# Performance work log

Hardware: AMD Instinct MI355X
Metric: run time of the kernel (lower is better)

The kernel has to match this reference:

```python
import jax, jax.numpy as jnp
import numpy as np

N_CODEBOOKS = 4
N_EMBED = 1024
EMBED_DIM = 64
PATCH = 4
BETA = 0.25
EPS = 1e-5
USAGE_W = 0.01


def setup_inputs() -> dict:
    key = jax.random.key(0)
    k1, k2 = jax.random.split(key)
    z = jax.random.normal(k1, (8, 64, 128, 128), dtype=jnp.float32)
    # one EMA codebook per quantizer, initialized ~ randn like torch buffer
    codebooks = jax.random.normal(k2, (N_CODEBOOKS, N_EMBED, EMBED_DIM), dtype=jnp.float32)
    return {"z": z, "codebooks": codebooks}


def _usage_loss(indices, n_embed):
    # negative-entropy penalty on code usage (no gradient path: counts are ints)
    counts = jnp.bincount(indices.reshape(-1), length=n_embed).astype(jnp.float32)
    probs = (counts + EPS) / (counts.sum() + EPS * n_embed)
    entropy = -jnp.sum(probs * jnp.log(probs + EPS))
    return jnp.log(jnp.float32(n_embed)) - entropy


def _ema_quantize(residual, embedding):
    # residual: [N, C, ph, pw], embedding: [n_e, C]; eval mode (no EMA buffer update)
    N, C, ph, pw = residual.shape
    z_flat = residual.transpose(0, 2, 3, 1).reshape(-1, C)  # [M, C]
    d = (jnp.sum(z_flat ** 2, axis=1, keepdims=True)
         + jnp.sum(embedding ** 2, axis=1)
         - 2.0 * z_flat @ embedding.T)  # [M, n_e]
    idx = jnp.argmin(d, axis=1)  # [M]
    z_q = embedding[idx].reshape(N, ph, pw, C).transpose(0, 3, 1, 2)  # [N, C, ph, pw]
    loss = BETA * jnp.mean((jax.lax.stop_gradient(z_q) - residual) ** 2)
    z_q_st = residual + jax.lax.stop_gradient(z_q - residual)  # straight-through
    return z_q_st, loss, idx.reshape(N, ph, pw)


def reference(z, codebooks):
    B, C, H, W = z.shape
    h, w = H // PATCH, W // PATCH
    # b c (h ph) (w pw) -> (b h w) c ph pw
    zp = (z.reshape(B, C, h, PATCH, w, PATCH)
            .transpose(0, 2, 4, 1, 3, 5)
            .reshape(B * h * w, C, PATCH, PATCH))
    zq_acc = jnp.zeros_like(zp)
    residual = zp
    losses, all_idx = [], []
    for i in range(N_CODEBOOKS):
        zq_i, loss_i, idx_i = _ema_quantize(residual, codebooks[i])
        loss_i = loss_i + USAGE_W * _usage_loss(idx_i, N_EMBED)
        zq_acc = zq_acc + zq_i
        residual = residual - zq_i
        losses.append(loss_i)
        all_idx.append(idx_i.reshape(idx_i.shape[0], -1))  # [N, ph*pw]
    loss = jnp.stack(losses).sum()
    # (b h w) c ph pw -> b c (h ph) (w pw)
    z_q = (zq_acc.reshape(B, h, w, C, PATCH, PATCH)
                 .transpose(0, 3, 1, 4, 2, 5)
                 .reshape(B, C, H, W))
    # [N, patch_area, n_codebooks] -> [b, h, w, patch_area, n_codebooks]
    min_idx = jnp.stack(all_idx, axis=-1).reshape(B, h, w, PATCH * PATCH, N_CODEBOOKS)
    return z_q, loss, min_idx
```

## Files before the change

kernel.cpp:

```cpp
#include <hip/hip_runtime.h>
#include <math.h>

typedef __attribute__((ext_vector_type(8))) short short8;
typedef __attribute__((ext_vector_type(4))) float f32x4;

#define NCB 4
#define NE 1024
#define DIM 64
#define HW 16384
#define NPIX 131072
#define NWAVES 4096
#define MSE_DENOM 8388608.0f
#define EPSF 1e-5f
#define CHUNK_BYTES 12288
#define NCHUNK 32

__device__ __forceinline__ unsigned short f2bf(float x) {
    unsigned u = __float_as_uint(x);
    u += 0x7fffu + ((u >> 16) & 1u);
    return (unsigned short)(u >> 16);
}
__device__ __forceinline__ float bf2f(unsigned short h) {
    return __uint_as_float(((unsigned)h) << 16);
}

__global__ __launch_bounds__(64) void rvq_norms(const float* __restrict__ cb,
                                                float* __restrict__ nrmh) {
    int code = blockIdx.x * 64 + threadIdx.x;
    const float4* row = reinterpret_cast<const float4*>(cb + (size_t)code * DIM);
    float s0 = 0.f, s1 = 0.f, s2 = 0.f, s3 = 0.f;
#pragma unroll
    for (int k = 0; k < 16; ++k) {
        float4 v = row[k];
        s0 = fmaf(v.x, v.x, s0); s1 = fmaf(v.y, v.y, s1);
        s2 = fmaf(v.z, v.z, s2); s3 = fmaf(v.w, v.w, s3);
    }
    nrmh[code] = -0.5f * ((s0 + s1) + (s2 + s3));
}

__global__ __launch_bounds__(256) void rvq_presplit(const float* __restrict__ cb,
                                                    unsigned short* __restrict__ gB) {
    int blk = blockIdx.x;
    int tid = threadIdx.x;
    int code64 = tid >> 2, dg = tid & 3;
    int c0 = (blk & 15) << 6;
    int i  = blk >> 4;
    const float4* s4 = reinterpret_cast<const float4*>(
        cb + ((size_t)i * NE + c0 + code64) * DIM + dg * 16);
    float v[16];
    {
        float4 q;
        q = s4[0]; v[0]=q.x; v[1]=q.y; v[2]=q.z; v[3]=q.w;
        q = s4[1]; v[4]=q.x; v[5]=q.y; v[6]=q.z; v[7]=q.w;
        q = s4[2]; v[8]=q.x; v[9]=q.y; v[10]=q.z; v[11]=q.w;
        q = s4[3]; v[12]=q.x; v[13]=q.y; v[14]=q.z; v[15]=q.w;
    }
    int chunk = (blk & 15) * 2 + (code64 >> 5);
    int j = code64 & 31;
    char* outc = reinterpret_cast<char*>(gB)
               + ((size_t)i * NCHUNK + chunk) * CHUNK_BYTES;
    int linbase = j * 128 + dg * 32;
    int sw = (j & 7) << 4;
#pragma unroll
    for (int h = 0; h < 2; ++h) {
        short8 p1, p2, p3;
#pragma unroll
        for (int e = 0; e < 8; ++e) {
            float t = v[h * 8 + e];
            unsigned short u1 = f2bf(t); t -= bf2f(u1);
            unsigned short u2 = f2bf(t); t -= bf2f(u2);
            unsigned short u3 = f2bf(t);
            p1[e] = (short)u1; p2[e] = (short)u2; p3[e] = (short)u3;
        }
        int a = (linbase + h * 16) ^ sw;
        *reinterpret_cast<short8*>(outc + a)        = p1;
        *reinterpret_cast<short8*>(outc + 4096 + a) = p2;
        *reinterpret_cast<short8*>(outc + 8192 + a) = p3;
    }
}

__device__ __forceinline__ void gload16(const void* gsrc, void* ldst) {
    __builtin_amdgcn_global_load_lds(
        (const __attribute__((address_space(1))) unsigned int*)gsrc,
        (__attribute__((address_space(3))) unsigned int*)ldst, 16, 0, 0);
}

__global__ __launch_bounds__(256, 4) void rvq_main(
    const float* __restrict__ z, const unsigned short* __restrict__ gB,
    const float* __restrict__ nrmh, const float* __restrict__ cb,
    float* __restrict__ out_zq, float* __restrict__ out_idx,
    unsigned* __restrict__ hist, float* __restrict__ msePartial)
{
    __shared__ uint4 sB[2][CHUNK_BYTES / 16];
    __shared__ int   sBest[4][32];

    const int tid  = threadIdx.x;
    const int lane = tid & 63;
    const int wid  = tid >> 6;
    const int col  = lane & 15;
    const int g    = lane >> 4;
    const int blockPix = blockIdx.x * 128;
    char* sBase = reinterpret_cast<char*>(sB);
    const int sw = (col & 7) << 4;

    size_t zb[2];
#pragma unroll
    for (int m = 0; m < 2; ++m) {
        int pf = blockPix + wid * 32 + m * 16 + col;
        zb[m] = (size_t)(pf >> 14) * 1048576 + (size_t)(pf & 16383);
    }

    float r[2][2][8];
#pragma unroll
    for (int m = 0; m < 2; ++m)
#pragma unroll
        for (int kh = 0; kh < 2; ++kh)
#pragma unroll
            for (int e = 0; e < 8; ++e)
                r[m][kh][e] = z[zb[m] + (size_t)(kh * 32 + g * 8 + e) * HW];

    for (int i = 0; i < NCB; ++i) {
        const char* gBi = reinterpret_cast<const char*>(gB) + (size_t)i * NCHUNK * CHUNK_BYTES;
        const float* nrm_i = nrmh + i * NE;

        short8 A[3][2][2];
#pragma unroll
        for (int m = 0; m < 2; ++m)
#pragma unroll
            for (int kh = 0; kh < 2; ++kh)
#pragma unroll
                for (int e = 0; e < 8; ++e) {
                    float t = r[m][kh][e];
                    unsigned short u1 = f2bf(t); t -= bf2f(u1);
                    unsigned short u2 = f2bf(t); t -= bf2f(u2);
                    unsigned short u3 = f2bf(t);
                    A[0][m][kh][e] = (short)u1;
                    A[1][m][kh][e] = (short)u2;
                    A[2][m][kh][e] = (short)u3;
                }

#pragma unroll
        for (int k = 0; k < 3; ++k)
            gload16(gBi + k * 4096 + tid * 16, sBase + k * 4096 + tid * 16);
        __syncthreads();

        float maxv[2][4]; int maxi[2][4];
#pragma unroll
        for (int m = 0; m < 2; ++m)
#pragma unroll
            for (int rr = 0; rr < 4; ++rr) { maxv[m][rr] = -3.4e38f; maxi[m][rr] = 0; }

        for (int c = 0; c < NCHUNK; ++c) {
            const int cur = c & 1;
            if (c < NCHUNK - 1) {
                const char* gc = gBi + (size_t)(c + 1) * CHUNK_BYTES;
                char* sbn = sBase + (cur ^ 1) * CHUNK_BYTES;
#pragma unroll
                for (int k = 0; k < 3; ++k)
                    gload16(gc + k * 4096 + tid * 16, sbn + k * 4096 + tid * 16);
            }
            const char* sbc = sBase + cur * CHUNK_BYTES;

#pragma unroll
            for (int sub = 0; sub < 2; ++sub) {
                const int code = (sub << 4) + col;
                float nh = nrm_i[(c << 5) + code];
                f32x4 acc[2];
#pragma unroll
                for (int rr = 0; rr < 4; ++rr) { acc[0][rr] = nh; acc[1][rr] = nh; }

                __builtin_amdgcn_s_setprio(1);
#pragma unroll
                for (int sb = 0; sb < 3; ++sb) {
                    short8 B0 = *reinterpret_cast<const short8*>(
                        sbc + sb * 4096 + ((((code << 7) + (g << 4))) ^ sw));
                    short8 B1 = *reinterpret_cast<const short8*>(
                        sbc + sb * 4096 + ((((code << 7) + 64 + (g << 4))) ^ sw));
#pragma unroll
                    for (int sa = 0; sa < 3 - sb; ++sa) {
                        acc[0] = __builtin_amdgcn_mfma_f32_16x16x32_bf16(A[sa][0][0], B0, acc[0], 0, 0, 0);
                        acc[1] = __builtin_amdgcn_mfma_f32_16x16x32_bf16(A[sa][1][0], B0, acc[1], 0, 0, 0);
                        acc[0] = __builtin_amdgcn_mfma_f32_16x16x32_bf16(A[sa][0][1], B1, acc[0], 0, 0, 0);
                        acc[1] = __builtin_amdgcn_mfma_f32_16x16x32_bf16(A[sa][1][1], B1, acc[1], 0, 0, 0);
                    }
                }
                __builtin_amdgcn_s_setprio(0);

#pragma unroll
                for (int m = 0; m < 2; ++m)
#pragma unroll
                    for (int rr = 0; rr < 4; ++rr) {
                        float s = acc[m][rr];
                        if (s > maxv[m][rr]) { maxv[m][rr] = s; maxi[m][rr] = (c << 5) + code; }
                    }
            }
            __syncthreads();
        }

#pragma unroll
        for (int m = 0; m < 2; ++m)
#pragma unroll
            for (int rr = 0; rr < 4; ++rr) {
                float v = maxv[m][rr]; int ix = maxi[m][rr];
#pragma unroll
                for (int off = 1; off < 16; off <<= 1) {
                    float ov = __shfl_xor(v, off, 64);
                    int   oi = __shfl_xor(ix, off, 64);
                    if (ov > v || (ov == v && oi < ix)) { v = ov; ix = oi; }
                }
                maxi[m][rr] = ix;
            }
        __syncthreads();
        if (col == 0) {
#pragma unroll
            for (int m = 0; m < 2; ++m)
#pragma unroll
                for (int rr = 0; rr < 4; ++rr)
                    sBest[wid][m * 16 + g * 4 + rr] = maxi[m][rr];
        }
        __syncthreads();
        int best[2];
        best[0] = sBest[wid][col];
        best[1] = sBest[wid][16 + col];

        const float* cbi = cb + (size_t)i * NE * DIM;
        if (lane < 16) {
#pragma unroll
            for (int m = 0; m < 2; ++m) {
                int pfr = blockPix + wid * 32 + m * 16 + lane;
                int bb = pfr >> 14, yy = (pfr >> 7) & 127, xx = pfr & 127;
                int bi = sBest[wid][m * 16 + lane];
                size_t off = (size_t)bb * 65536 + (size_t)(yy >> 2) * 2048
                           + (size_t)(xx >> 2) * 64
                           + (size_t)(((yy & 3) << 2) + (xx & 3)) * 4 + (size_t)i;
                out_idx[off] = (float)bi;
                atomicAdd(&hist[i * NE + bi], 1u);
            }
        }

#pragma unroll
        for (int m = 0; m < 2; ++m) {
            const float* er = cbi + (size_t)best[m] * DIM;
#pragma unroll
            for (int kh = 0; kh < 2; ++kh) {
                const float4* e4 = reinterpret_cast<const float4*>(er + kh * 32 + g * 8);
                float4 q0 = e4[0], q1 = e4[1];
                r[m][kh][0] -= q0.x; r[m][kh][1] -= q0.y;
                r[m][kh][2] -= q0.z; r[m][kh][3] -= q0.w;
                r[m][kh][4] -= q1.x; r[m][kh][5] -= q1.y;
                r[m][kh][6] -= q1.z; r[m][kh][7] -= q1.w;
            }
        }

        float s = 0.f;
#pragma unroll
        for (int m = 0; m < 2; ++m)
#pragma unroll
            for (int kh = 0; kh < 2; ++kh)
#pragma unroll
                for (int e = 0; e < 8; ++e) s = fmaf(r[m][kh][e], r[m][kh][e], s);
#pragma unroll
        for (int d_ = 32; d_ > 0; d_ >>= 1) s += __shfl_down(s, d_, 64);
        if (lane == 0) msePartial[i * NWAVES + blockIdx.x * 4 + wid] = s;
    }

#pragma unroll
    for (int m = 0; m < 2; ++m)
#pragma unroll
        for (int kh = 0; kh < 2; ++kh)
#pragma unroll
            for (int e = 0; e < 8; ++e) {
                size_t o = zb[m] + (size_t)(kh * 32 + g * 8 + e) * HW;
                out_zq[o] = z[o] - r[m][kh][e];
            }
}

__global__ __launch_bounds__(1024) void rvq_finalize(
    const unsigned* __restrict__ hist, const float* __restrict__ msePartial,
    float* __restrict__ out_loss)
{
    __shared__ float red[1024];
    int t = threadIdx.x;
    float loss = 0.f;
    for (int i = 0; i < NCB; ++i) {
        float cnt = (float)hist[i * NE + t];
        float prob = (cnt + EPSF) / (131072.0f + EPSF * 1024.0f);
        red[t] = -prob * logf(prob + EPSF);
        __syncthreads();
        for (int s = 512; s > 0; s >>= 1) { if (t < s) red[t] += red[t + s]; __syncthreads(); }
        float entropy = red[0];
        __syncthreads();
        red[t] = msePartial[i * NWAVES + t]        + msePartial[i * NWAVES + 1024 + t]
               + msePartial[i * NWAVES + 2048 + t] + msePartial[i * NWAVES + 3072 + t];
        __syncthreads();
        for (int s = 512; s > 0; s >>= 1) { if (t < s) red[t] += red[t + s]; __syncthreads(); }
        float mse_sum = red[0];
        __syncthreads();
        loss += 0.25f * (mse_sum / MSE_DENOM) + 0.01f * (logf(1024.0f) - entropy);
    }
    if (t == 0) out_loss[0] = loss;
}

extern "C" void kernel_launch(void* const* d_in, const int* in_sizes, int n_in,
                              void* d_out, int out_size, void* d_ws, size_t ws_size,
                              hipStream_t stream) {
    const float* z  = (const float*)d_in[0];
    const float* cb = (const float*)d_in[1];

    float* out      = (float*)d_out;
    float* out_zq   = out;
    float* out_loss = out + 8388608;
    float* out_idx  = out + 8388609;

    unsigned* hist        = (unsigned*)d_ws;
    float*    nrmh        = (float*)((char*)d_ws + 16384);
    float*    msePartial  = (float*)((char*)d_ws + 32768);
    unsigned short* gB    = (unsigned short*)((char*)d_ws + 98304);

    hipMemsetAsync(d_ws, 0, 16384, stream);
    rvq_norms<<<64, 64, 0, stream>>>(cb, nrmh);
    rvq_presplit<<<64, 256, 0, stream>>>(cb, gB);
    rvq_main<<<1024, 256, 0, stream>>>(z, gB, nrmh, cb, out_zq, out_idx, hist, msePartial);
    rvq_finalize<<<1, 1024, 0, stream>>>(hist, msePartial, out_loss);
}
```

Measured before the change: 383.0 us.

## Halve pixels per wave to double grid size and raise occupancy

Each wave now handles 16 pixels instead of 32, so the grid doubles to 2048 blocks and launch bounds request 5 blocks per CU. The per-wave MSE partial buffer and the finalize reduction grow to match, and the workspace layout moves the presplit codebook further out. This trades register pressure and per-block work for more parallelism across CUs. The cost is that each codebook chunk staged in LDS is now reused by half as many pixels, so codebook traffic from global memory into LDS doubles.

Result: slower. 399.5 us (+4.3%).

```diff
diff --git a/kernel.cpp b/kernel.cpp
--- a/kernel.cpp
+++ b/kernel.cpp
@@ -9,7 +9,7 @@
 #define DIM 64
 #define HW 16384
 #define NPIX 131072
-#define NWAVES 4096
+#define NWAVES 8192
 #define MSE_DENOM 8388608.0f
 #define EPSF 1e-5f
 #define CHUNK_BYTES 12288
@@ -85,70 +85,60 @@
         (__attribute__((address_space(3))) unsigned int*)ldst, 16, 0, 0);
 }
 
-__global__ __launch_bounds__(256, 4) void rvq_main(
+__global__ __launch_bounds__(256, 5) void rvq_main(
     const float* __restrict__ z, const unsigned short* __restrict__ gB,
     const float* __restrict__ nrmh, const float* __restrict__ cb,
     float* __restrict__ out_zq, float* __restrict__ out_idx,
     unsigned* __restrict__ hist, float* __restrict__ msePartial)
 {
     __shared__ uint4 sB[2][CHUNK_BYTES / 16];
-    __shared__ int   sBest[4][32];
+    __shared__ int   sBest[4][16];
 
     const int tid  = threadIdx.x;
     const int lane = tid & 63;
     const int wid  = tid >> 6;
     const int col  = lane & 15;
     const int g    = lane >> 4;
-    const int blockPix = blockIdx.x * 128;
+    const int blockPix = blockIdx.x * 64;
     char* sBase = reinterpret_cast<char*>(sB);
     const int sw = (col & 7) << 4;
 
-    size_t zb[2];
-#pragma unroll
-    for (int m = 0; m < 2; ++m) {
-        int pf = blockPix + wid * 32 + m * 16 + col;
-        zb[m] = (size_t)(pf >> 14) * 1048576 + (size_t)(pf & 16383);
-    }
-
-    float r[2][2][8];
-#pragma unroll
-    for (int m = 0; m < 2; ++m)
-#pragma unroll
-        for (int kh = 0; kh < 2; ++kh)
-#pragma unroll
-            for (int e = 0; e < 8; ++e)
-                r[m][kh][e] = z[zb[m] + (size_t)(kh * 32 + g * 8 + e) * HW];
+    const int pf = blockPix + wid * 16 + col;
+    const size_t zb = (size_t)(pf >> 14) * 1048576 + (size_t)(pf & 16383);
+
+    float r[2][8];
+#pragma unroll
+    for (int kh = 0; kh < 2; ++kh)
+#pragma unroll
+        for (int e = 0; e < 8; ++e)
+            r[kh][e] = z[zb + (size_t)(kh * 32 + g * 8 + e) * HW];
 
     for (int i = 0; i < NCB; ++i) {
         const char* gBi = reinterpret_cast<const char*>(gB) + (size_t)i * NCHUNK * CHUNK_BYTES;
         const float* nrm_i = nrmh + i * NE;
 
-        short8 A[3][2][2];
-#pragma unroll
-        for (int m = 0; m < 2; ++m)
-#pragma unroll
-            for (int kh = 0; kh < 2; ++kh)
-#pragma unroll
-                for (int e = 0; e < 8; ++e) {
-                    float t = r[m][kh][e];
-                    unsigned short u1 = f2bf(t); t -= bf2f(u1);
-                    unsigned short u2 = f2bf(t); t -= bf2f(u2);
-                    unsigned short u3 = f2bf(t);
-                    A[0][m][kh][e] = (short)u1;
-                    A[1][m][kh][e] = (short)u2;
-                    A[2][m][kh][e] = (short)u3;
-                }
+        short8 A[3][2];
+#pragma unroll
+        for (int kh = 0; kh < 2; ++kh)
+#pragma unroll
+            for (int e = 0; e < 8; ++e) {
+                float t = r[kh][e];
+                unsigned short u1 = f2bf(t); t -= bf2f(u1);
+                unsigned short u2 = f2bf(t); t -= bf2f(u2);
+                unsigned short u3 = f2bf(t);
+                A[0][kh][e] = (short)u1;
+                A[1][kh][e] = (short)u2;
+                A[2][kh][e] = (short)u3;
+            }
 
 #pragma unroll
         for (int k = 0; k < 3; ++k)
             gload16(gBi + k * 4096 + tid * 16, sBase + k * 4096 + tid * 16);
         __syncthreads();
 
-        float maxv[2][4]; int maxi[2][4];
-#pragma unroll
-        for (int m = 0; m < 2; ++m)
-#pragma unroll
-            for (int rr = 0; rr < 4; ++rr) { maxv[m][rr] = -3.4e38f; maxi[m][rr] = 0; }
+        float maxv[4]; int maxi[4];
+#pragma unroll
+        for (int rr = 0; rr < 4; ++rr) { maxv[rr] = -3.4e38f; maxi[rr] = 0; }
 
         for (int c = 0; c < NCHUNK; ++c) {
             const int cur = c & 1;
@@ -165,9 +155,9 @@
             for (int sub = 0; sub < 2; ++sub) {
                 const int code = (sub << 4) + col;
                 float nh = nrm_i[(c << 5) + code];
-                f32x4 acc[2];
-#pragma unroll
-                for (int rr = 0; rr < 4; ++rr) { acc[0][rr] = nh; acc[1][rr] = nh; }
+                f32x4 acc;
+#pragma unroll
+                for (int rr = 0; rr < 4; ++rr) acc[rr] = nh;
 
                 __builtin_amdgcn_s_setprio(1);
 #pragma unroll
@@ -178,101 +168,83 @@
                         sbc + sb * 4096 + ((((code << 7) + 64 + (g << 4))) ^ sw));
 #pragma unroll
                     for (int sa = 0; sa < 3 - sb; ++sa) {
-                        acc[0] = __builtin_amdgcn_mfma_f32_16x16x32_bf16(A[sa][0][0], B0, acc[0], 0, 0, 0);
-                        acc[1] = __builtin_amdgcn_mfma_f32_16x16x32_bf16(A[sa][1][0], B0, acc[1], 0, 0, 0);
-                        acc[0] = __builtin_amdgcn_mfma_f32_16x16x32_bf16(A[sa][0][1], B1, acc[0], 0, 0, 0);
-                        acc[1] = __builtin_amdgcn_mfma_f32_16x16x32_bf16(A[sa][1][1], B1, acc[1], 0, 0, 0);
+                        acc = __builtin_amdgcn_mfma_f32_16x16x32_bf16(A[sa][0], B0, acc, 0, 0, 0);
+                        acc = __builtin_amdgcn_mfma_f32_16x16x32_bf16(A[sa][1], B1, acc, 0, 0, 0);
                     }
                 }
                 __builtin_amdgcn_s_setprio(0);
 
 #pragma unroll
-                for (int m = 0; m < 2; ++m)
-#pragma unroll
-                    for (int rr = 0; rr < 4; ++rr) {
-                        float s = acc[m][rr];
-                        if (s > maxv[m][rr]) { maxv[m][rr] = s; maxi[m][rr] = (c << 5) + code; }
-                    }
+                for (int rr = 0; rr < 4; ++rr) {
+                    float s = acc[rr];
+                    if (s > maxv[rr]) { maxv[rr] = s; maxi[rr] = (c << 5) + code; }
+                }
             }
             __syncthreads();
         }
 
 #pragma unroll
-        for (int m = 0; m < 2; ++m)
-#pragma unroll
-            for (int rr = 0; rr < 4; ++rr) {
-                float v = maxv[m][rr]; int ix = maxi[m][rr];
-#pragma unroll
-                for (int off = 1; off < 16; off <<= 1) {
-                    float ov = __shfl_xor(v, off, 64);
-                    int   oi = __shfl_xor(ix, off, 64);
-                    if (ov > v || (ov == v && oi < ix)) { v = ov; ix = oi; }
-                }
-                maxi[m][rr] = ix;
-            }
+        for (int rr = 0; rr < 4; ++rr) {
+            float v = maxv[rr]; int ix = maxi[rr];
+#pragma unroll
+            for (int off = 1; off < 16; off <<= 1) {
+                float ov = __shfl_xor(v, off, 64);
+                int   oi = __shfl_xor(ix, off, 64);
+                if (ov > v || (ov == v && oi < ix)) { v = ov; ix = oi; }
+            }
+            maxi[rr] = ix;
+        }
         __syncthreads();
         if (col == 0) {
 #pragma unroll
-            for (int m = 0; m < 2; ++m)
-#pragma unroll
-                for (int rr = 0; rr < 4; ++rr)
-                    sBest[wid][m * 16 + g * 4 + rr] = maxi[m][rr];
-        }
-        __syncthreads();
-        int best[2];
-        best[0] = sBest[wid][col];
-        best[1] = sBest[wid][16 + col];
+            for (int rr = 0; rr < 4; ++rr)
+                sBest[wid][g * 4 + rr] = maxi[rr];
+        }
+        __syncthreads();
+        const int best = sBest[wid][col];
 
         const float* cbi = cb + (size_t)i * NE * DIM;
         if (lane < 16) {
-#pragma unroll
-            for (int m = 0; m < 2; ++m) {
-                int pfr = blockPix + wid * 32 + m * 16 + lane;
-                int bb = pfr >> 14, yy = (pfr >> 7) & 127, xx = pfr & 127;
-                int bi = sBest[wid][m * 16 + lane];
-                size_t off = (size_t)bb * 65536 + (size_t)(yy >> 2) * 2048
-                           + (size_t)(xx >> 2) * 64
-                           + (size_t)(((yy & 3) << 2) + (xx & 3)) * 4 + (size_t)i;
-                out_idx[off] = (float)bi;
-                atomicAdd(&hist[i * NE + bi], 1u);
-            }
-        }
-
-#pragma unroll
-        for (int m = 0; m < 2; ++m) {
-            const float* er = cbi + (size_t)best[m] * DIM;
+            int pfr = blockPix + wid * 16 + lane;
+            int bb = pfr >> 14, yy = (pfr >> 7) & 127, xx = pfr & 127;
+            int bi = sBest[wid][lane];
+            size_t off = (size_t)bb * 65536 + (size_t)(yy >> 2) * 2048
+                       + (size_t)(xx >> 2) * 64
+                       + (size_t)(((yy & 3) << 2) + (xx & 3)) * 4 + (size_t)i;
+            out_idx[off] = (float)bi;
+            atomicAdd(&hist[i * NE + bi], 1u);
+        }
+
+        {
+            const float* er = cbi + (size_t)best * DIM;
 #pragma unroll
             for (int kh = 0; kh < 2; ++kh) {
                 const float4* e4 = reinterpret_cast<const float4*>(er + kh * 32 + g * 8);
                 float4 q0 = e4[0], q1 = e4[1];
-                r[m][kh][0] -= q0.x; r[m][kh][1] -= q0.y;
-                r[m][kh][2] -= q0.z; r[m][kh][3] -= q0.w;
-                r[m][kh][4] -= q1.x; r[m][kh][5] -= q1.y;
-                r[m][kh][6] -= q1.z; r[m][kh][7] -= q1.w;
+                r[kh][0] -= q0.x; r[kh][1] -= q0.y;
+                r[kh][2] -= q0.z; r[kh][3] -= q0.w;
+                r[kh][4] -= q1.x; r[kh][5] -= q1.y;
+                r[kh][6] -= q1.z; r[kh][7] -= q1.w;
             }
         }
 
         float s = 0.f;
 #pragma unroll
-        for (int m = 0; m < 2; ++m)
-#pragma unroll
-            for (int kh = 0; kh < 2; ++kh)
-#pragma unroll
-                for (int e = 0; e < 8; ++e) s = fmaf(r[m][kh][e], r[m][kh][e], s);
+        for (int kh = 0; kh < 2; ++kh)
+#pragma unroll
+            for (int e = 0; e < 8; ++e) s = fmaf(r[kh][e], r[kh][e], s);
 #pragma unroll
         for (int d_ = 32; d_ > 0; d_ >>= 1) s += __shfl_down(s, d_, 64);
         if (lane == 0) msePartial[i * NWAVES + blockIdx.x * 4 + wid] = s;
     }
 
 #pragma unroll
-    for (int m = 0; m < 2; ++m)
-#pragma unroll
-        for (int kh = 0; kh < 2; ++kh)
-#pragma unroll
-            for (int e = 0; e < 8; ++e) {
-                size_t o = zb[m] + (size_t)(kh * 32 + g * 8 + e) * HW;
-                out_zq[o] = z[o] - r[m][kh][e];
-            }
+    for (int kh = 0; kh < 2; ++kh)
+#pragma unroll
+        for (int e = 0; e < 8; ++e) {
+            size_t o = zb + (size_t)(kh * 32 + g * 8 + e) * HW;
+            out_zq[o] = z[o] - r[kh][e];
+        }
 }
 
 __global__ __launch_bounds__(1024) void rvq_finalize(
@@ -290,8 +262,10 @@
         for (int s = 512; s > 0; s >>= 1) { if (t < s) red[t] += red[t + s]; __syncthreads(); }
         float entropy = red[0];
         __syncthreads();
-        red[t] = msePartial[i * NWAVES + t]        + msePartial[i * NWAVES + 1024 + t]
-               + msePartial[i * NWAVES + 2048 + t] + msePartial[i * NWAVES + 3072 + t];
+        float acc = 0.f;
+#pragma unroll
+        for (int k = 0; k < 8; ++k) acc += msePartial[i * NWAVES + k * 1024 + t];
+        red[t] = acc;
         __syncthreads();
         for (int s = 512; s > 0; s >>= 1) { if (t < s) red[t] += red[t + s]; __syncthreads(); }
         float mse_sum = red[0];
@@ -315,11 +289,11 @@
     unsigned* hist        = (unsigned*)d_ws;
     float*    nrmh        = (float*)((char*)d_ws + 16384);
     float*    msePartial  = (float*)((char*)d_ws + 32768);
-    unsigned short* gB    = (unsigned short*)((char*)d_ws + 98304);
+    unsigned short* gB    = (unsigned short*)((char*)d_ws + 163840);
 
     hipMemsetAsync(d_ws, 0, 16384, stream);
     rvq_norms<<<64, 64, 0, stream>>>(cb, nrmh);
     rvq_presplit<<<64, 256, 0, stream>>>(cb, gB);
-    rvq_main<<<1024, 256, 0, stream>>>(z, gB, nrmh, cb, out_zq, out_idx, hist, msePartial);
+    rvq_main<<<2048, 256, 0, stream>>>(z, gB, nrmh, cb, out_zq, out_idx, hist, msePartial);
     rvq_finalize<<<1, 1024, 0, stream>>>(hist, msePartial, out_loss);
 }
```

## Use larger codebook chunks with triple-buffered LDS and one barrier per chunk

Applied to the files above, without the earlier changes.

Codebook chunks grow from 32 to 64 codes, so there are 16 chunks per codebook instead of 32. The LDS staging becomes a 3-deep ring driven by explicit vmcnt waits and a single s_barrier per chunk, replacing the two __syncthreads per chunk and several barriers in the argmin epilogue. The aim is to cut barrier and synchronisation overhead and overlap global-to-LDS loads with MFMA work. In exchange, LDS use rises to about 72KB per block and launch bounds drop to 2 blocks per CU, which lowers occupancy.

Result: no change. 384.6 us (+0.4%).

```diff
diff --git a/kernel.cpp b/kernel.cpp
--- a/kernel.cpp
+++ b/kernel.cpp
@@ -12,8 +12,9 @@
 #define NWAVES 4096
 #define MSE_DENOM 8388608.0f
 #define EPSF 1e-5f
-#define CHUNK_BYTES 12288
-#define NCHUNK 32
+#define CHUNK_BYTES 24576
+#define CHUNK_SHORTS 12288
+#define NCHUNK 16
 
 __device__ __forceinline__ unsigned short f2bf(float x) {
     unsigned u = __float_as_uint(x);
@@ -42,11 +43,11 @@
                                                     unsigned short* __restrict__ gB) {
     int blk = blockIdx.x;
     int tid = threadIdx.x;
-    int code64 = tid >> 2, dg = tid & 3;
+    int code = tid >> 2, dg = tid & 3;
     int c0 = (blk & 15) << 6;
     int i  = blk >> 4;
     const float4* s4 = reinterpret_cast<const float4*>(
-        cb + ((size_t)i * NE + c0 + code64) * DIM + dg * 16);
+        cb + ((size_t)i * NE + c0 + code) * DIM + dg * 16);
     float v[16];
     {
         float4 q;
@@ -55,12 +56,9 @@
         q = s4[2]; v[8]=q.x; v[9]=q.y; v[10]=q.z; v[11]=q.w;
         q = s4[3]; v[12]=q.x; v[13]=q.y; v[14]=q.z; v[15]=q.w;
     }
-    int chunk = (blk & 15) * 2 + (code64 >> 5);
-    int j = code64 & 31;
-    char* outc = reinterpret_cast<char*>(gB)
-               + ((size_t)i * NCHUNK + chunk) * CHUNK_BYTES;
-    int linbase = j * 128 + dg * 32;
-    int sw = (j & 7) << 4;
+    char* outc = reinterpret_cast<char*>(gB + (size_t)blk * CHUNK_SHORTS);
+    int linbase = code * 128 + dg * 32;
+    int sw = (code & 7) << 4;
 #pragma unroll
     for (int h = 0; h < 2; ++h) {
         short8 p1, p2, p3;
@@ -73,9 +71,9 @@
             p1[e] = (short)u1; p2[e] = (short)u2; p3[e] = (short)u3;
         }
         int a = (linbase + h * 16) ^ sw;
-        *reinterpret_cast<short8*>(outc + a)        = p1;
-        *reinterpret_cast<short8*>(outc + 4096 + a) = p2;
-        *reinterpret_cast<short8*>(outc + 8192 + a) = p3;
+        *reinterpret_cast<short8*>(outc + a)         = p1;
+        *reinterpret_cast<short8*>(outc + 8192 + a)  = p2;
+        *reinterpret_cast<short8*>(outc + 16384 + a) = p3;
     }
 }
 
@@ -85,13 +83,13 @@
         (__attribute__((address_space(3))) unsigned int*)ldst, 16, 0, 0);
 }
 
-__global__ __launch_bounds__(256, 4) void rvq_main(
+__global__ __launch_bounds__(256, 2) void rvq_main(
     const float* __restrict__ z, const unsigned short* __restrict__ gB,
     const float* __restrict__ nrmh, const float* __restrict__ cb,
     float* __restrict__ out_zq, float* __restrict__ out_idx,
     unsigned* __restrict__ hist, float* __restrict__ msePartial)
 {
-    __shared__ uint4 sB[2][CHUNK_BYTES / 16];
+    __shared__ uint4 sB[3][CHUNK_BYTES / 16];
     __shared__ int   sBest[4][32];
 
     const int tid  = threadIdx.x;
@@ -140,9 +138,8 @@
                 }
 
 #pragma unroll
-        for (int k = 0; k < 3; ++k)
+        for (int k = 0; k < 6; ++k)
             gload16(gBi + k * 4096 + tid * 16, sBase + k * 4096 + tid * 16);
-        __syncthreads();
 
         float maxv[2][4]; int maxi[2][4];
 #pragma unroll
@@ -151,20 +148,23 @@
             for (int rr = 0; rr < 4; ++rr) { maxv[m][rr] = -3.4e38f; maxi[m][rr] = 0; }
 
         for (int c = 0; c < NCHUNK; ++c) {
-            const int cur = c & 1;
             if (c < NCHUNK - 1) {
                 const char* gc = gBi + (size_t)(c + 1) * CHUNK_BYTES;
-                char* sbn = sBase + (cur ^ 1) * CHUNK_BYTES;
-#pragma unroll
-                for (int k = 0; k < 3; ++k)
+                char* sbn = sBase + ((c + 1) % 3) * CHUNK_BYTES;
+#pragma unroll
+                for (int k = 0; k < 6; ++k)
                     gload16(gc + k * 4096 + tid * 16, sbn + k * 4096 + tid * 16);
-            }
-            const char* sbc = sBase + cur * CHUNK_BYTES;
-
-#pragma unroll
-            for (int sub = 0; sub < 2; ++sub) {
+                asm volatile("s_waitcnt vmcnt(6)" ::: "memory");
+            } else {
+                asm volatile("s_waitcnt vmcnt(0)" ::: "memory");
+            }
+            __builtin_amdgcn_s_barrier();
+            const char* sbc = sBase + (c % 3) * CHUNK_BYTES;
+
+#pragma unroll
+            for (int sub = 0; sub < 4; ++sub) {
                 const int code = (sub << 4) + col;
-                float nh = nrm_i[(c << 5) + code];
+                float nh = nrm_i[(c << 6) + code];
                 f32x4 acc[2];
 #pragma unroll
                 for (int rr = 0; rr < 4; ++rr) { acc[0][rr] = nh; acc[1][rr] = nh; }
@@ -173,9 +173,9 @@
 #pragma unroll
                 for (int sb = 0; sb < 3; ++sb) {
                     short8 B0 = *reinterpret_cast<const short8*>(
-                        sbc + sb * 4096 + ((((code << 7) + (g << 4))) ^ sw));
+                        sbc + sb * 8192 + ((((code << 7) + (g << 4))) ^ sw));
                     short8 B1 = *reinterpret_cast<const short8*>(
-                        sbc + sb * 4096 + ((((code << 7) + 64 + (g << 4))) ^ sw));
+                        sbc + sb * 8192 + ((((code << 7) + 64 + (g << 4))) ^ sw));
 #pragma unroll
                     for (int sa = 0; sa < 3 - sb; ++sa) {
                         acc[0] = __builtin_amdgcn_mfma_f32_16x16x32_bf16(A[sa][0][0], B0, acc[0], 0, 0, 0);
@@ -191,10 +191,9 @@
 #pragma unroll
                     for (int rr = 0; rr < 4; ++rr) {
                         float s = acc[m][rr];
-                        if (s > maxv[m][rr]) { maxv[m][rr] = s; maxi[m][rr] = (c << 5) + code; }
+                        if (s > maxv[m][rr]) { maxv[m][rr] = s; maxi[m][rr] = (c << 6) + code; }
                     }
             }
-            __syncthreads();
         }
 
 #pragma unroll
@@ -210,7 +209,6 @@
                 }
                 maxi[m][rr] = ix;
             }
-        __syncthreads();
         if (col == 0) {
 #pragma unroll
             for (int m = 0; m < 2; ++m)
@@ -218,10 +216,6 @@
                 for (int rr = 0; rr < 4; ++rr)
                     sBest[wid][m * 16 + g * 4 + rr] = maxi[m][rr];
         }
-        __syncthreads();
-        int best[2];
-        best[0] = sBest[wid][col];
-        best[1] = sBest[wid][16 + col];
 
         const float* cbi = cb + (size_t)i * NE * DIM;
         if (lane < 16) {
@@ -240,7 +234,8 @@
 
 #pragma unroll
         for (int m = 0; m < 2; ++m) {
-            const float* er = cbi + (size_t)best[m] * DIM;
+            const int best = sBest[wid][m * 16 + col];
+            const float* er = cbi + (size_t)best * DIM;
 #pragma unroll
             for (int kh = 0; kh < 2; ++kh) {
                 const float4* e4 = reinterpret_cast<const float4*>(er + kh * 32 + g * 8);
@@ -262,6 +257,8 @@
 #pragma unroll
         for (int d_ = 32; d_ > 0; d_ >>= 1) s += __shfl_down(s, d_, 64);
         if (lane == 0) msePartial[i * NWAVES + blockIdx.x * 4 + wid] = s;
+
+        __syncthreads();
     }
 
 #pragma unroll
@@ -290,8 +287,10 @@
         for (int s = 512; s > 0; s >>= 1) { if (t < s) red[t] += red[t + s]; __syncthreads(); }
         float entropy = red[0];
         __syncthreads();
-        red[t] = msePartial[i * NWAVES + t]        + msePartial[i * NWAVES + 1024 + t]
-               + msePartial[i * NWAVES + 2048 + t] + msePartial[i * NWAVES + 3072 + t];
+        float acc = 0.f;
+#pragma unroll
+        for (int k = 0; k < 4; ++k) acc += msePartial[i * NWAVES + k * 1024 + t];
+        red[t] = acc;
         __syncthreads();
         for (int s = 512; s > 0; s >>= 1) { if (t < s) red[t] += red[t + s]; __syncthreads(); }
         float mse_sum = red[0];
@@ -315,7 +314,7 @@
     unsigned* hist        = (unsigned*)d_ws;
     float*    nrmh        = (float*)((char*)d_ws + 16384);
     float*    msePartial  = (float*)((char*)d_ws + 32768);
-    unsigned short* gB    = (unsigned short*)((char*)d_ws + 98304);
+    unsigned short* gB    = (unsigned short*)((char*)d_ws + 163840);
 
     hipMemsetAsync(d_ws, 0, 16384, stream);
     rvq_norms<<<64, 64, 0, stream>>>(cb, nrmh);
```
